# Kernel optimization log

Hardware: AMD Instinct MI355X
Metric: run time of the kernel (lower is better)

Reference implementation:

```python
import jax, jax.numpy as jnp
import numpy as np


def setup_inputs() -> dict:
    key = jax.random.key(0)
    ks = jax.random.split(key, 24)
    N, E, D, A = 50000, 600000, 128, 128   # nodes, edges, in_dim(=out_dim), attn_dim
    NQ, NREL = 1024, 200
    NRE = 2 * NREL + 1                      # rela_embed rows
    s = 0.05

    def nrm(k, shape):
        return jax.random.normal(k, shape, jnp.float32) * s

    # edges columns: [query_idx, unused, rel, unused, sub, obj]
    r_idx = jax.random.randint(ks[0], (E,), 0, NQ, jnp.int32)
    rel = jax.random.randint(ks[1], (E,), 0, NRE, jnp.int32)
    sub = jax.random.randint(ks[2], (E,), 0, N, jnp.int32)
    # guarantee every node appears as an obj so the softmax denominator is never 0
    obj = jnp.concatenate([jnp.arange(N, dtype=jnp.int32),
                           jax.random.randint(ks[3], (E - N,), 0, N, jnp.int32)])
    zc = jnp.zeros((E,), jnp.int32)
    edges = jnp.stack([r_idx, zc, rel, zc, sub, obj], axis=1)

    q_rel = jax.random.randint(ks[4], (NQ,), 0, NRE, jnp.int32)
    hidden = jax.random.normal(ks[5], (N, D), jnp.float32)

    return {
        "hidden": hidden,
        "rela_embed": nrm(ks[6], (NRE, D)),
        # GateUnit (GRU-style gate over x=[h_r; h_qr] with state h_s)
        "Wz": nrm(ks[7], (2 * D, D)), "Uz": nrm(ks[8], (D, D)), "bz": jnp.zeros((D,), jnp.float32),
        "Wr_g": nrm(ks[9], (2 * D, D)), "Ur": nrm(ks[10], (D, D)), "br": jnp.zeros((D,), jnp.float32),
        "Whh": nrm(ks[11], (2 * D, D)), "Uh": nrm(ks[12], (D, D)), "bh": jnp.zeros((D,), jnp.float32),
        # attention
        "Ws_attn": nrm(ks[13], (D, A)),
        "Wqr_attn": nrm(ks[14], (D, A)), "b_qr": jnp.zeros((A,), jnp.float32),
        "w_alpha": nrm(ks[15], (A, 1)), "b_alpha": jnp.zeros((1,), jnp.float32),
        # output projection
        "W_h": nrm(ks[16], (D, D)),
        "q_rel": q_rel,
        "edges": edges,
        "n_node": N,
    }


def gate_unit(h_r, h_qr, h_s, Wz, Uz, bz, Wr_g, Ur, br, Whh, Uh, bh):
    # GRU-style gated update: x = [h_r; h_qr], state = h_s
    x = jnp.concatenate([h_r, h_qr], axis=-1)
    z = jax.nn.sigmoid(x @ Wz + h_s @ Uz + bz)
    r = jax.nn.sigmoid(x @ Wr_g + h_s @ Ur + br)
    h_tilde = jnp.tanh(x @ Whh + (r * h_s) @ Uh + bh)
    return (1.0 - z) * h_s + z * h_tilde


def reference(hidden, rela_embed, Wz, Uz, bz, Wr_g, Ur, br, Whh, Uh, bh,
              Ws_attn, Wqr_attn, b_qr, w_alpha, b_alpha, W_h,
              q_rel, edges, n_node):
    r_idx = edges[:, 0]   # query index per edge
    rel = edges[:, 2]
    sub = edges[:, 4]
    obj = edges[:, 5]

    h_s = hidden[sub]               # [E, D] gather
    h_r = rela_embed[rel]           # [E, D]
    hq = rela_embed[q_rel]          # [NQ, D]
    h_qr = hq[r_idx]                # [E, D]

    # node_group[obj] = r_idx (duplicate writes: last-write semantics, as torch)
    node_group = jnp.zeros((n_node,), dtype=edges.dtype).at[obj].set(r_idx)
    h_n_qr = hq[node_group]         # [n_node, D]

    message = gate_unit(h_r, h_qr, h_s, Wz, Uz, bz, Wr_g, Ur, br, Whh, Uh, bh)  # [E, D]

    attn = jax.nn.relu(message @ Ws_attn + h_qr @ Wqr_attn + b_qr) @ w_alpha + b_alpha  # [E, 1]
    exp_a = jnp.exp(attn)

    sum_exp = jax.ops.segment_sum(exp_a, obj, num_segments=n_node)             # [n_node, 1]
    agg = jax.ops.segment_sum(exp_a * message, obj, num_segments=n_node)       # [n_node, D]
    message_agg = agg / sum_exp

    hidden_new = jax.nn.relu(message_agg @ W_h)
    return hidden_new, h_n_qr
```

## Files before the change

### kernel.cpp

```cpp
#include <hip/hip_runtime.h>
#include <hip/hip_bf16.h>

#define D 128

typedef unsigned int u32;
typedef unsigned short ushort_t;

typedef __attribute__((ext_vector_type(8))) __bf16 bf16x8;
typedef __attribute__((ext_vector_type(4))) float f32x4;

__device__ __forceinline__ float bf2f(ushort_t u){ return __uint_as_float(((u32)u)<<16); }
__device__ __forceinline__ ushort_t f2bf(float f){
  u32 x = __float_as_uint(f);
  return (ushort_t)((x + 0x7fffu + ((x>>16)&1u)) >> 16);
}
__device__ __forceinline__ float2 bfp2(u32 w){
  float2 r; r.x = __uint_as_float(w<<16); r.y = __uint_as_float(w & 0xffff0000u); return r;
}
__device__ __forceinline__ u32 packbf(float a, float b){
  return (u32)f2bf(a) | ((u32)f2bf(b)<<16);
}
__device__ __forceinline__ u32 cvtpk(float a, float b){
  u32 r; asm("v_cvt_pk_bf16_f32 %0, %1, %2" : "=v"(r) : "v"(a), "v"(b)); return r;
}
__device__ __forceinline__ ushort_t cvt1(float a){
  u32 r; asm("v_cvt_pk_bf16_f32 %0, %1, %1" : "=v"(r) : "v"(a)); return (ushort_t)r;
}
__device__ __forceinline__ void atompk(ushort_t* p, u32 v){
  asm volatile("global_atomic_pk_add_bf16 %0, %1, off" :: "v"(p), "v"(v) : "memory");
}
__device__ __forceinline__ float sigm(float x){ return 1.0f/(1.0f+__expf(-x)); }
__device__ __forceinline__ float ftanh(float x){
  float e = __expf(-2.0f*fabsf(x));
  float t = (1.0f-e)/(1.0f+e);
  return copysignf(t,x);
}

__global__ void detect_kernel(const u32* __restrict__ words, int* flag){
  int t = threadIdx.x;
  int cnt = 0;
  for (int i = t; i < 512; i += 64){
    u32 w = words[i];
    u32 e = (w >> 7) & 0xFFu;
    if (e >= 100u && e <= 126u) cnt++;
  }
  #pragma unroll
  for (int off = 32; off > 0; off >>= 1) cnt += __shfl_xor(cnt, off);
  if (t == 0) *flag = (cnt < 256) ? 1 : 0;
}

struct CvtArgs { const void* src[17]; ushort_t* dst[17]; int n[17]; };

__global__ __launch_bounds__(256) void convert_kernel(CvtArgs a, const int* __restrict__ flag){
  int isf = *flag;
  int gid = blockIdx.x*blockDim.x + threadIdx.x;
  int gs  = gridDim.x*blockDim.x;
  for (int s = 0; s < 17; s++){
    int n = a.n[s];
    ushort_t* dst = a.dst[s];
    int n4 = n >> 2;
    if (isf){
      const float4* src4 = (const float4*)a.src[s];
      uint2* dst4 = (uint2*)dst;
      for (int j = gid; j < n4; j += gs){
        float4 v = src4[j];
        uint2 o; o.x = packbf(v.x, v.y); o.y = packbf(v.z, v.w);
        dst4[j] = o;
      }
      const float* src = (const float*)a.src[s];
      for (int j = (n4<<2) + gid; j < n; j += gs) dst[j] = f2bf(src[j]);
    } else {
      const uint2* src4 = (const uint2*)a.src[s];
      uint2* dst4 = (uint2*)dst;
      for (int j = gid; j < n4; j += gs) dst4[j] = src4[j];
      const ushort_t* src = (const ushort_t*)a.src[s];
      for (int j = (n4<<2) + gid; j < n; j += gs) dst[j] = src[j];
    }
  }
}

__global__ void init_kernel(u32* aggz, float* sum_exp, int* last_edge, int N){
  int i = blockIdx.x*blockDim.x + threadIdx.x;
  int stride = gridDim.x*blockDim.x;
  int na = N*D/2;
  int na4 = na >> 2;
  uint4 z4 = make_uint4(0,0,0,0);
  for (int j=i; j<na4; j+=stride) ((uint4*)aggz)[j] = z4;
  for (int j=(na4<<2)+i; j<na; j+=stride) aggz[j]=0u;
  for (int j=i; j<N;  j+=stride){ sum_exp[j]=0.f; last_edge[j]=-1; }
}

__global__ void table_kernel(const ushort_t* __restrict__ rela,
  const ushort_t* __restrict__ Wz, const ushort_t* __restrict__ Wr, const ushort_t* __restrict__ Wh,
  const ushort_t* __restrict__ Wqr,
  const ushort_t* __restrict__ bz, const ushort_t* __restrict__ br, const ushort_t* __restrict__ bh,
  const ushort_t* __restrict__ bqr,
  const int* __restrict__ q_rel,
  ushort_t* hq_tab, u32* __restrict__ RELP, u32* __restrict__ RIDP,
  ushort_t* CaT, int NRE, int NQ)
{
  __shared__ float hrow[D];
  int d = threadIdx.x;
  int b = blockIdx.x;
  if (b < NRE) {
    const ushort_t* row = rela + (size_t)b*D;
    hrow[d] = bf2f(row[d]);
    __syncthreads();
    float az=0.f, ar=0.f, ah=0.f;
    for (int k=0;k<D;k++){
      float h = hrow[k];
      az += h*bf2f(Wz[k*D+d]);
      ar += h*bf2f(Wr[k*D+d]);
      ah += h*bf2f(Wh[k*D+d]);
    }
    float azn = __shfl_xor(az,1), arn = __shfl_xor(ar,1), ahn = __shfl_xor(ah,1);
    if (!(d & 1)){
      u32* out = RELP + (size_t)b*192 + (d>>1)*3;
      out[0] = packbf(az, azn); out[1] = packbf(ar, arn); out[2] = packbf(ah, ahn);
    }
  } else {
    int q = b - NRE; if (q >= NQ) return;
    int rq = q_rel[q];
    const ushort_t* row = rela + (size_t)rq*D;
    hrow[d] = bf2f(row[d]);
    hq_tab[q*D+d] = row[d];
    __syncthreads();
    float vz=bf2f(bz[d]), vr=bf2f(br[d]), vh=bf2f(bh[d]), vc=bf2f(bqr[d]);
    for (int k=0;k<D;k++){
      float h = hrow[k];
      vz += h*bf2f(Wz[(D+k)*D+d]);
      vr += h*bf2f(Wr[(D+k)*D+d]);
      vh += h*bf2f(Wh[(D+k)*D+d]);
      vc += h*bf2f(Wqr[k*D+d]);
    }
    float vzn = __shfl_xor(vz,1), vrn = __shfl_xor(vr,1), vhn = __shfl_xor(vh,1);
    if (!(d & 1)){
      u32* out = RIDP + (size_t)q*192 + (d>>1)*3;
      out[0] = packbf(vz, vzn); out[1] = packbf(vr, vrn); out[2] = packbf(vh, vhn);
    }
    CaT[q*D + (d&15)*8 + (d>>4)] = f2bf(vc);
  }
}

__device__ __forceinline__ void matvec16(const char* vA_hi, const char* vA_lo,
                                         const char* Bm, int l, f32x4 acc[8])
{
  int arow = l & 15, agrp = l >> 4;
  int swz = (arow & 7) << 4;
  bf16x8 ah[4], al[4];
  #pragma unroll
  for (int kk=0; kk<4; kk++){
    int off = (kk*64 + agrp*16) ^ swz;
    ah[kk] = *(const bf16x8*)(vA_hi + arow*256 + off);
    al[kk] = *(const bf16x8*)(vA_lo + arow*256 + off);
  }
  #pragma unroll
  for (int t=0; t<8; t++){
    const char* bbase = Bm + (t*16 + arow)*256;
    #pragma unroll
    for (int kk=0; kk<4; kk++){
      bf16x8 bf = *(const bf16x8*)(bbase + ((kk*64 + agrp*16) ^ swz));
      acc[t] = __builtin_amdgcn_mfma_f32_16x16x32_bf16(ah[kk], bf, acc[t], 0,0,0);
      acc[t] = __builtin_amdgcn_mfma_f32_16x16x32_bf16(al[kk], bf, acc[t], 0,0,0);
    }
  }
}

__device__ __forceinline__ void matvec16s(const char* vA,
                                          const char* Bm, int l, f32x4 acc[8])
{
  int arow = l & 15, agrp = l >> 4;
  int swz = (arow & 7) << 4;
  bf16x8 ah[4];
  #pragma unroll
  for (int kk=0; kk<4; kk++){
    int off = (kk*64 + agrp*16) ^ swz;
    ah[kk] = *(const bf16x8*)(vA + arow*256 + off);
  }
  #pragma unroll
  for (int t=0; t<8; t++){
    const char* bbase = Bm + (t*16 + arow)*256;
    #pragma unroll
    for (int kk=0; kk<4; kk++){
      bf16x8 bf = *(const bf16x8*)(bbase + ((kk*64 + agrp*16) ^ swz));
      acc[t] = __builtin_amdgcn_mfma_f32_16x16x32_bf16(ah[kk], bf, acc[t], 0,0,0);
    }
  }
}

#define HU_SMEM (65536 + 8*8192)

__global__ __launch_bounds__(512, 2) void hu_kernel(
  const ushort_t* __restrict__ hidden,
  const ushort_t* __restrict__ Uz, const ushort_t* __restrict__ Ur,
  u32* __restrict__ SUB3, int N)
{
  extern __shared__ char smem[];
  int tid = threadIdx.x;
  int w = tid >> 6, l = tid & 63;

  for (int idx = tid; idx < 128*64; idx += 512) {
    int k  = idx >> 6;
    int cp = idx & 63;
    u32 wu = *(const u32*)(Uz + (size_t)k*D + 2*cp);
    u32 ww = *(const u32*)(Ur + (size_t)k*D + 2*cp);
    int r0 = 2*cp, r1 = 2*cp+1;
    int o0 = (2*k) ^ ((r0&7)<<4);
    int o1 = (2*k) ^ ((r1&7)<<4);
    *(ushort_t*)(smem + r0*256 + o0) = (ushort_t)(wu & 0xffffu);
    *(ushort_t*)(smem + r1*256 + o1) = (ushort_t)(wu >> 16);
    *(ushort_t*)(smem + 32768 + r0*256 + o0) = (ushort_t)(ww & 0xffffu);
    *(ushort_t*)(smem + 32768 + r1*256 + o1) = (ushort_t)(ww >> 16);
  }
  __syncthreads();

  char* vA  = smem + 65536 + w*8192;
  u32* accb = (u32*)vA;
  int arow = l & 15, agrp = l >> 4;
  int c0 = 2*l;

  int nIter = (N + 127) >> 7;
  for (int it = blockIdx.x; it < nIter; it += gridDim.x) {
    int base = it*128 + w*16;
    u32 hword[16];
    #pragma unroll
    for (int e=0;e<16;e++){
      int n = base + e; if (n >= N) n = N-1;
      u32 hw = *(const u32*)(hidden + (size_t)n*D + c0);
      hword[e] = hw;
      *(u32*)(vA + e*256 + ((4*l) ^ ((e&7)<<4))) = hw;
    }
    f32x4 az[8], ar[8];
    #pragma unroll
    for (int t=0;t<8;t++){ az[t]=(f32x4){0.f,0.f,0.f,0.f}; ar[t]=(f32x4){0.f,0.f,0.f,0.f}; }
    matvec16s(vA, smem, l, az);
    matvec16s(vA, smem + 32768, l, ar);

    #pragma unroll
    for (int t=0;t<8;t++){
      #pragma unroll
      for (int r=0;r<4;r++){
        int e_ = agrp*4 + r;
        int c  = t*16 + arow;
        accb[e_*128 + (c ^ (agrp<<3))] = __float_as_uint(az[t][r]);
      }
    }
    float2 xz[16];
    #pragma unroll
    for (int e=0;e<16;e++)
      xz[e] = *(float2*)&accb[e*128 + ((2*l) ^ ((e>>2)<<3))];
    #pragma unroll
    for (int t=0;t<8;t++){
      #pragma unroll
      for (int r=0;r<4;r++){
        int e_ = agrp*4 + r;
        int c  = t*16 + arow;
        accb[e_*128 + (c ^ (agrp<<3))] = __float_as_uint(ar[t][r]);
      }
    }
    float2 xr[16];
    #pragma unroll
    for (int e=0;e<16;e++)
      xr[e] = *(float2*)&accb[e*128 + ((2*l) ^ ((e>>2)<<3))];

    #pragma unroll
    for (int e=0;e<16;e++){
      int n = base + e;
      if (n < N){
        u32* out = SUB3 + (size_t)n*192 + l*3;
        out[0] = packbf(xz[e].x, xz[e].y);
        out[1] = packbf(xr[e].x, xr[e].y);
        out[2] = hword[e];
      }
    }
  }
}

#define SMEM_WST 32768
#define SMEM_VA  65536
#define EDGE_SMEM (65536 + 8*8192)

__global__ __launch_bounds__(512, 2) void edge_kernel(
  const int* __restrict__ edges,
  const u32* __restrict__ SUB3, const u32* __restrict__ RELP, const u32* __restrict__ RIDP,
  const ushort_t* __restrict__ CaT,
  const ushort_t* __restrict__ Uh, const ushort_t* __restrict__ Ws,
  const ushort_t* __restrict__ w_alpha, const ushort_t* __restrict__ b_alpha,
  ushort_t* __restrict__ aggh, float* __restrict__ sum_exp, int* __restrict__ last_edge,
  int E)
{
  extern __shared__ char smem[];
  int tid = threadIdx.x;
  int w = tid >> 6, l = tid & 63;

  for (int idx = tid; idx < 128*64; idx += 512) {
    int k  = idx >> 6;
    int cp = idx & 63;
    u32 wu = *(const u32*)(Uh + (size_t)k*D + 2*cp);
    u32 ww = *(const u32*)(Ws + (size_t)k*D + 2*cp);
    int r0 = 2*cp, r1 = 2*cp+1;
    int o0 = (2*k) ^ ((r0&7)<<4);
    int o1 = (2*k) ^ ((r1&7)<<4);
    *(ushort_t*)(smem + r0*256 + o0) = (ushort_t)(wu & 0xffffu);
    *(ushort_t*)(smem + r1*256 + o1) = (ushort_t)(wu >> 16);
    *(ushort_t*)(smem + SMEM_WST + r0*256 + o0) = (ushort_t)(ww & 0xffffu);
    *(ushort_t*)(smem + SMEM_WST + r1*256 + o1) = (ushort_t)(ww >> 16);
  }
  __syncthreads();

  char* vA_hi = smem + SMEM_VA + w*8192;
  char* vA_lo = vA_hi + 4096;
  u32*  accb  = (u32*)vA_hi;

  int arow = l & 15, agrp = l >> 4;
  float wal[8];
  #pragma unroll
  for (int t=0; t<8; t++) wal[t] = bf2f(w_alpha[t*16 + arow]);
  float bal = bf2f(b_alpha[0]);
  int c0 = 2*l;

  int nIter = (E + 127) >> 7;
  for (int it = blockIdx.x; it < nIter; it += gridDim.x) {
    int eb = it*128 + w*16;

    int myE = eb + arow; if (myE >= E) myE = E - 1;
    const int* ep = edges + (size_t)myE*6;
    int v_ridx = ep[0];
    int v_rel  = ep[2];
    int v_sub  = ep[4];
    int v_obj  = ep[5];

    u32 zpk[16], hwd[16], acp[16];
    #pragma unroll
    for (int e=0; e<16; e++){
      int rel = __shfl(v_rel, e);
      int rid = __shfl(v_ridx, e);
      int sub = __shfl(v_sub, e);
      uint3 rp = *(const uint3*)(RELP + (size_t)rel*192 + l*3);
      uint3 qp = *(const uint3*)(RIDP + (size_t)rid*192 + l*3);
      uint3 sp = *(const uint3*)(SUB3 + (size_t)sub*192 + l*3);
      float2 az = bfp2(rp.x), ar = bfp2(rp.y), ah = bfp2(rp.z);
      float2 bz = bfp2(qp.x), br = bfp2(qp.y), bh = bfp2(qp.z);
      float2 hz = bfp2(sp.x), hr = bfp2(sp.y), hs = bfp2(sp.z);
      float z0 = sigm(az.x+bz.x+hz.x), z1 = sigm(az.y+bz.y+hz.y);
      float r0 = sigm(ar.x+br.x+hr.x), r1 = sigm(ar.y+br.y+hr.y);
      float v0 = r0*hs.x, v1 = r1*hs.y;
      u32 u0 = __float_as_uint(v0), u1 = __float_as_uint(v1);
      u32 whi = (u0 >> 16) | (u1 & 0xffff0000u);
      float vl0 = v0 - __uint_as_float(u0 & 0xffff0000u);
      float vl1 = v1 - __uint_as_float(u1 & 0xffff0000u);
      int voff = e*256 + ((4*l) ^ ((e&7)<<4));
      *(u32*)(vA_hi + voff) = whi;
      *(u32*)(vA_lo + voff) = cvtpk(vl0, vl1);
      zpk[e] = cvtpk(z0, z1);
      hwd[e] = sp.z;
      acp[e] = cvtpk(ah.x+bh.x, ah.y+bh.y);
    }

    f32x4 acc[8];
    #pragma unroll
    for (int t=0; t<8; t++) acc[t] = (f32x4){0.f,0.f,0.f,0.f};
    matvec16(vA_hi, vA_lo, smem, l, acc);

    #pragma unroll
    for (int t=0; t<8; t++){
      #pragma unroll
      for (int r=0; r<4; r++){
        int e_ = agrp*4 + r;
        int c  = t*16 + arow;
        accb[e_*128 + (c ^ (agrp<<3))] = __float_as_uint(acc[t][r]);
      }
    }
    float2 xv[16];
    #pragma unroll
    for (int e=0; e<16; e++)
      xv[e] = *(float2*)&accb[e*128 + ((2*l) ^ ((e>>2)<<3))];

    float mf0[16], mf1[16];
    #pragma unroll
    for (int e=0; e<16; e++){
      float2 ac = bfp2(acp[e]);
      float2 zh = bfp2(zpk[e]);
      float2 hs = bfp2(hwd[e]);
      float ht0 = ftanh(xv[e].x + ac.x);
      float ht1 = ftanh(xv[e].y + ac.y);
      float m0 = (1.0f - zh.x)*hs.x + zh.x*ht0;
      float m1 = (1.0f - zh.y)*hs.y + zh.y*ht1;
      mf0[e] = m0; mf1[e] = m1;
      u32 u0 = __float_as_uint(m0), u1 = __float_as_uint(m1);
      u32 whi = (u0 >> 16) | (u1 & 0xffff0000u);
      float vl0 = m0 - __uint_as_float(u0 & 0xffff0000u);
      float vl1 = m1 - __uint_as_float(u1 & 0xffff0000u);
      int voff = e*256 + ((4*l) ^ ((e&7)<<4));
      *(u32*)(vA_hi + voff) = whi;
      *(u32*)(vA_lo + voff) = cvtpk(vl0, vl1);
    }

    f32x4 a2[8];
    #pragma unroll
    for (int t=0; t<8; t++) a2[t] = (f32x4){0.f,0.f,0.f,0.f};
    matvec16(vA_hi, vA_lo, smem + SMEM_WST, l, a2);

    float ea[4];
    #pragma unroll
    for (int r=0; r<4; r++){
      int rid_r = __shfl(v_ridx, agrp*4 + r);
      uint4 cw = *(const uint4*)(CaT + (size_t)rid_r*D + arow*8);
      float2 c01 = bfp2(cw.x), c23 = bfp2(cw.y), c45 = bfp2(cw.z), c67 = bfp2(cw.w);
      float s = 0.f;
      s += fmaxf(a2[0][r]+c01.x,0.f)*wal[0];
      s += fmaxf(a2[1][r]+c01.y,0.f)*wal[1];
      s += fmaxf(a2[2][r]+c23.x,0.f)*wal[2];
      s += fmaxf(a2[3][r]+c23.y,0.f)*wal[3];
      s += fmaxf(a2[4][r]+c45.x,0.f)*wal[4];
      s += fmaxf(a2[5][r]+c45.y,0.f)*wal[5];
      s += fmaxf(a2[6][r]+c67.x,0.f)*wal[6];
      s += fmaxf(a2[7][r]+c67.y,0.f)*wal[7];
      s += __shfl_xor(s, 1); s += __shfl_xor(s, 2);
      s += __shfl_xor(s, 4); s += __shfl_xor(s, 8);
      ea[r] = __expf(s + bal);
    }

    #pragma unroll
    for (int e=0; e<16; e++){
      float ea_e = __shfl(ea[e & 3], (e >> 2) << 4);
      int obj_e  = __shfl(v_obj, e);
      int eg = eb + e;
      if (eg < E)
        atompk(aggh + (size_t)obj_e*D + c0, cvtpk(ea_e*mf0[e], ea_e*mf1[e]));
    }
    {
      int srcl = (arow >> 2) << 4;
      float s0 = __shfl(ea[0], srcl);
      float s1 = __shfl(ea[1], srcl);
      float s2 = __shfl(ea[2], srcl);
      float s3 = __shfl(ea[3], srcl);
      int rr = arow & 3;
      float eav = (rr == 0) ? s0 : (rr == 1) ? s1 : (rr == 2) ? s2 : s3;
      if (agrp == 0 && (eb + arow) < E){
        atomicAdd(sum_exp + v_obj, eav);
        atomicMax(last_edge + v_obj, eb + arow);
      }
    }
  }
}

__global__ __launch_bounds__(256) void final_kernel(
  const ushort_t* __restrict__ aggh, const float* __restrict__ sum_exp,
  const int* __restrict__ last_edge, const int* __restrict__ edges,
  const ushort_t* __restrict__ hq_tab, const ushort_t* __restrict__ Wh,
  const int* __restrict__ flag, void* __restrict__ out_base, int N)
{
  __shared__ float mb[4][D][4];
  int tid = threadIdx.x, w = tid >> 6, l = tid & 63;
  int c0 = 2*l, c1 = c0+1;
  int isf = *flag;
  float* out0f = (float*)out_base;
  float* out1f = out0f + (size_t)N*D;
  ushort_t* out0h = (ushort_t*)out_base;
  ushort_t* out1h = out0h + (size_t)N*D;
  int nIter = (N + 15) >> 4;
  for (int it = blockIdx.x; it < nIter; it += gridDim.x){
    int base = it*16 + w*4;
    int rq[4];
    #pragma unroll
    for (int e=0;e<4;e++){
      int n = base + e; if (n >= N) n = N-1;
      float se = sum_exp[n];
      float inv = (se > 0.f) ? (1.0f/se) : 0.f;
      float2 m = bfp2(*(const u32*)(aggh + (size_t)n*D + c0));
      mb[w][c0][e] = m.x*inv; mb[w][c1][e] = m.y*inv;
      int le = last_edge[n];
      rq[e] = (le >= 0) ? edges[(size_t)le*6] : 0;
    }
    float a0[4] = {0,0,0,0}, a1[4] = {0,0,0,0};
    #pragma unroll 4
    for (int kp=0; kp<64; kp++){
      float4 ma = *(float4*)&mb[w][2*kp][0];
      float4 mv = *(float4*)&mb[w][2*kp+1][0];
      float2 u0 = bfp2(*(const u32*)(Wh + (2*kp)*D + c0));
      float2 u1 = bfp2(*(const u32*)(Wh + (2*kp+1)*D + c0));
      a0[0] += ma.x*u0.x + mv.x*u1.x;  a1[0] += ma.x*u0.y + mv.x*u1.y;
      a0[1] += ma.y*u0.x + mv.y*u1.x;  a1[1] += ma.y*u0.y + mv.y*u1.y;
      a0[2] += ma.z*u0.x + mv.z*u1.x;  a1[2] += ma.z*u0.y + mv.z*u1.y;
      a0[3] += ma.w*u0.x + mv.w*u1.x;  a1[3] += ma.w*u0.y + mv.w*u1.y;
    }
    #pragma unroll
    for (int e=0;e<4;e++){
      int n = base + e; if (n >= N) continue;
      float r0 = fmaxf(a0[e], 0.f), r1 = fmaxf(a1[e], 0.f);
      u32 hqw = *(const u32*)(hq_tab + (size_t)rq[e]*D + c0);
      if (isf){
        float2 o0; o0.x = r0; o0.y = r1;
        *(float2*)(out0f + (size_t)n*D + c0) = o0;
        float2 hv = bfp2(hqw);
        *(float2*)(out1f + (size_t)n*D + c0) = hv;
      } else {
        *(u32*)(out0h + (size_t)n*D + c0) = packbf(r0, r1);
        *(u32*)(out1h + (size_t)n*D + c0) = hqw;
      }
    }
  }
}

extern "C" void kernel_launch(void* const* d_in, const int* in_sizes, int n_in,
                              void* d_out, int out_size, void* d_ws, size_t ws_size,
                              hipStream_t stream)
{
  const int* q_rel = (const int*)d_in[17];
  const int* edges = (const int*)d_in[18];

  int N   = in_sizes[0]/D;
  int NRE = in_sizes[1]/D;
  int NQ  = in_sizes[17];
  int E   = in_sizes[18]/6;

  char* ws = (char*)d_ws;
  size_t o = 0;
  auto alloc = [&](size_t bytes)->void*{
    void* p = ws + o; o += (bytes + 255) & ~(size_t)255; return p;
  };
  ushort_t* aggh  = (ushort_t*)alloc((size_t)N*D*2);
  float* sum_exp  = (float*)alloc((size_t)N*4);
  int*   lastedge = (int*)  alloc((size_t)N*4);
  int*   flag     = (int*)  alloc(256);

  ushort_t* canon[17];
  for (int i=0;i<17;i++) canon[i] = (ushort_t*)alloc((size_t)in_sizes[i]*2);

  ushort_t* hq_tab = (ushort_t*)alloc((size_t)NQ*D*2);
  ushort_t* CaT = (ushort_t*)alloc((size_t)NQ*D*2);
  u32* RELP = (u32*)alloc((size_t)NRE*192*4);
  u32* RIDP = (u32*)alloc((size_t)NQ*192*4);
  u32* SUB3 = (u32*)alloc((size_t)N*192*4);

  CvtArgs ca;
  for (int i=0;i<17;i++){ ca.src[i]=d_in[i]; ca.dst[i]=canon[i]; ca.n[i]=in_sizes[i]; }

  const ushort_t* hidden = canon[0];
  const ushort_t* rela   = canon[1];
  const ushort_t* Wz  = canon[2];
  const ushort_t* Uz  = canon[3];
  const ushort_t* bz  = canon[4];
  const ushort_t* Wr  = canon[5];
  const ushort_t* Ur  = canon[6];
  const ushort_t* br  = canon[7];
  const ushort_t* Whh = canon[8];
  const ushort_t* Uh  = canon[9];
  const ushort_t* bh  = canon[10];
  const ushort_t* Ws  = canon[11];
  const ushort_t* Wqr = canon[12];
  const ushort_t* bqr = canon[13];
  const ushort_t* wal = canon[14];
  const ushort_t* bal = canon[15];
  const ushort_t* W_h = canon[16];

  detect_kernel<<<1, 64, 0, stream>>>((const u32*)d_in[1], flag);
  convert_kernel<<<1024, 256, 0, stream>>>(ca, flag);
  init_kernel<<<4096, 256, 0, stream>>>((u32*)aggh, sum_exp, lastedge, N);
  table_kernel<<<NRE+NQ, 128, 0, stream>>>(rela, Wz, Wr, Whh, Wqr, bz, br, bh, bqr,
                                           q_rel, hq_tab, RELP, RIDP, CaT, NRE, NQ);

  hipFuncSetAttribute(reinterpret_cast<const void*>(hu_kernel),
                      hipFuncAttributeMaxDynamicSharedMemorySize, HU_SMEM);
  hu_kernel<<<256, 512, HU_SMEM, stream>>>(hidden, Uz, Ur, SUB3, N);

  hipFuncSetAttribute(reinterpret_cast<const void*>(edge_kernel),
                      hipFuncAttributeMaxDynamicSharedMemorySize, EDGE_SMEM);
  edge_kernel<<<256, 512, EDGE_SMEM, stream>>>(edges, SUB3, RELP, RIDP, CaT,
                                               Uh, Ws, wal, bal, aggh, sum_exp, lastedge, E);
  final_kernel<<<1024, 256, 0, stream>>>(aggh, sum_exp, lastedge, edges, hq_tab, W_h,
                                         flag, d_out, N);
}
```

Measured before the change: 619.3 us.

## Raise edge and hu kernels to 768-thread blocks and fuse detect/init into convert

The hu and edge kernels now launch 12 waves per block instead of 8, with per-wave LDS scratch grown to match and each iteration covering 192 rows or edges instead of 128. The aim is more resident waves to hide gather latency. The launch bounds tighten the per-thread register budget, which risks spills in the register-heavy edge kernel, and LDS use rises to 160KB per block. Separately, the dtype-detection and buffer-zeroing kernels are folded into the convert kernel, saving two launches. Each convert block now recomputes the detection flag itself.

```diff
diff --git a/kernel.cpp b/kernel.cpp
--- a/kernel.cpp
+++ b/kernel.cpp
@@ -36,24 +36,31 @@
   return copysignf(t,x);
 }
 
-__global__ void detect_kernel(const u32* __restrict__ words, int* flag){
-  int t = threadIdx.x;
-  int cnt = 0;
-  for (int i = t; i < 512; i += 64){
-    u32 w = words[i];
-    u32 e = (w >> 7) & 0xFFu;
-    if (e >= 100u && e <= 126u) cnt++;
-  }
-  #pragma unroll
-  for (int off = 32; off > 0; off >>= 1) cnt += __shfl_xor(cnt, off);
-  if (t == 0) *flag = (cnt < 256) ? 1 : 0;
-}
-
 struct CvtArgs { const void* src[17]; ushort_t* dst[17]; int n[17]; };
 
-__global__ __launch_bounds__(256) void convert_kernel(CvtArgs a, const int* __restrict__ flag){
-  int isf = *flag;
-  int gid = blockIdx.x*blockDim.x + threadIdx.x;
+__global__ __launch_bounds__(256) void convert_kernel(CvtArgs a,
+  const u32* __restrict__ probe, int* __restrict__ flag,
+  u32* __restrict__ aggz, float* __restrict__ sum_exp, int* __restrict__ last_edge, int N)
+{
+  __shared__ int s_isf;
+  int tid = threadIdx.x;
+  if (tid < 64){
+    int cnt = 0;
+    for (int i = tid; i < 512; i += 64){
+      u32 w = probe[i];
+      u32 e = (w >> 7) & 0xFFu;
+      if (e >= 100u && e <= 126u) cnt++;
+    }
+    #pragma unroll
+    for (int off = 32; off > 0; off >>= 1) cnt += __shfl_xor(cnt, off);
+    if (tid == 0){
+      s_isf = (cnt < 256) ? 1 : 0;
+      if (blockIdx.x == 0) *flag = s_isf;
+    }
+  }
+  __syncthreads();
+  int isf = s_isf;
+  int gid = blockIdx.x*blockDim.x + tid;
   int gs  = gridDim.x*blockDim.x;
   for (int s = 0; s < 17; s++){
     int n = a.n[s];
@@ -77,17 +84,12 @@
       for (int j = (n4<<2) + gid; j < n; j += gs) dst[j] = src[j];
     }
   }
-}
-
-__global__ void init_kernel(u32* aggz, float* sum_exp, int* last_edge, int N){
-  int i = blockIdx.x*blockDim.x + threadIdx.x;
-  int stride = gridDim.x*blockDim.x;
   int na = N*D/2;
   int na4 = na >> 2;
   uint4 z4 = make_uint4(0,0,0,0);
-  for (int j=i; j<na4; j+=stride) ((uint4*)aggz)[j] = z4;
-  for (int j=(na4<<2)+i; j<na; j+=stride) aggz[j]=0u;
-  for (int j=i; j<N;  j+=stride){ sum_exp[j]=0.f; last_edge[j]=-1; }
+  for (int j=gid; j<na4; j+=gs) ((uint4*)aggz)[j] = z4;
+  for (int j=(na4<<2)+gid; j<na; j+=gs) aggz[j]=0u;
+  for (int j=gid; j<N;  j+=gs){ sum_exp[j]=0.f; last_edge[j]=-1; }
 }
 
 __global__ void table_kernel(const ushort_t* __restrict__ rela,
@@ -188,9 +190,9 @@
   }
 }
 
-#define HU_SMEM (65536 + 8*8192)
-
-__global__ __launch_bounds__(512, 2) void hu_kernel(
+#define HU_SMEM (65536 + 12*8192)
+
+__global__ __launch_bounds__(768, 3) void hu_kernel(
   const ushort_t* __restrict__ hidden,
   const ushort_t* __restrict__ Uz, const ushort_t* __restrict__ Ur,
   u32* __restrict__ SUB3, int N)
@@ -199,7 +201,7 @@
   int tid = threadIdx.x;
   int w = tid >> 6, l = tid & 63;
 
-  for (int idx = tid; idx < 128*64; idx += 512) {
+  for (int idx = tid; idx < 128*64; idx += 768) {
     int k  = idx >> 6;
     int cp = idx & 63;
     u32 wu = *(const u32*)(Uz + (size_t)k*D + 2*cp);
@@ -219,9 +221,9 @@
   int arow = l & 15, agrp = l >> 4;
   int c0 = 2*l;
 
-  int nIter = (N + 127) >> 7;
+  int nIter = (N + 191) / 192;
   for (int it = blockIdx.x; it < nIter; it += gridDim.x) {
-    int base = it*128 + w*16;
+    int base = it*192 + w*16;
     u32 hword[16];
     #pragma unroll
     for (int e=0;e<16;e++){
@@ -278,9 +280,9 @@
 
 #define SMEM_WST 32768
 #define SMEM_VA  65536
-#define EDGE_SMEM (65536 + 8*8192)
-
-__global__ __launch_bounds__(512, 2) void edge_kernel(
+#define EDGE_SMEM (65536 + 12*8192)
+
+__global__ __launch_bounds__(768, 3) void edge_kernel(
   const int* __restrict__ edges,
   const u32* __restrict__ SUB3, const u32* __restrict__ RELP, const u32* __restrict__ RIDP,
   const ushort_t* __restrict__ CaT,
@@ -293,7 +295,7 @@
   int tid = threadIdx.x;
   int w = tid >> 6, l = tid & 63;
 
-  for (int idx = tid; idx < 128*64; idx += 512) {
+  for (int idx = tid; idx < 128*64; idx += 768) {
     int k  = idx >> 6;
     int cp = idx & 63;
     u32 wu = *(const u32*)(Uh + (size_t)k*D + 2*cp);
@@ -319,9 +321,9 @@
   float bal = bf2f(b_alpha[0]);
   int c0 = 2*l;
 
-  int nIter = (E + 127) >> 7;
+  int nIter = (E + 191) / 192;
   for (int it = blockIdx.x; it < nIter; it += gridDim.x) {
-    int eb = it*128 + w*16;
+    int eb = it*192 + w*16;
 
     int myE = eb + arow; if (myE >= E) myE = E - 1;
     const int* ep = edges + (size_t)myE*6;
@@ -555,19 +557,18 @@
   const ushort_t* bal = canon[15];
   const ushort_t* W_h = canon[16];
 
-  detect_kernel<<<1, 64, 0, stream>>>((const u32*)d_in[1], flag);
-  convert_kernel<<<1024, 256, 0, stream>>>(ca, flag);
-  init_kernel<<<4096, 256, 0, stream>>>((u32*)aggh, sum_exp, lastedge, N);
+  convert_kernel<<<1024, 256, 0, stream>>>(ca, (const u32*)d_in[1], flag,
+                                           (u32*)aggh, sum_exp, lastedge, N);
   table_kernel<<<NRE+NQ, 128, 0, stream>>>(rela, Wz, Wr, Whh, Wqr, bz, br, bh, bqr,
                                            q_rel, hq_tab, RELP, RIDP, CaT, NRE, NQ);
 
   hipFuncSetAttribute(reinterpret_cast<const void*>(hu_kernel),
                       hipFuncAttributeMaxDynamicSharedMemorySize, HU_SMEM);
-  hu_kernel<<<256, 512, HU_SMEM, stream>>>(hidden, Uz, Ur, SUB3, N);
+  hu_kernel<<<256, 768, HU_SMEM, stream>>>(hidden, Uz, Ur, SUB3, N);
 
   hipFuncSetAttribute(reinterpret_cast<const void*>(edge_kernel),
                       hipFuncAttributeMaxDynamicSharedMemorySize, EDGE_SMEM);
-  edge_kernel<<<256, 512, EDGE_SMEM, stream>>>(edges, SUB3, RELP, RIDP, CaT,
+  edge_kernel<<<256, 768, EDGE_SMEM, stream>>>(edges, SUB3, RELP, RIDP, CaT,
                                                Uh, Ws, wal, bal, aggh, sum_exp, lastedge, E);
   final_kernel<<<1024, 256, 0, stream>>>(aggh, sum_exp, lastedge, edges, hq_tab, W_h,
                                          flag, d_out, N);
```

New measurement: 640.4 us. 1.03x slower.
